# Kernel tuning notes

Hardware: AMD Instinct MI355X
Metric: run time of the kernel (lower is better)

## Reference

```python
import jax, jax.numpy as jnp
import numpy as np

B, T, N, M = 128, 128, 128, 256  # batch, timesteps, driving series, hidden size


def setup_inputs() -> dict:
    key = jax.random.key(0)
    ks = jax.random.split(key, 8)
    def p(k, shape, fan):
        return jax.random.normal(k, shape, jnp.float32) / np.float32(np.sqrt(fan))
    X = jax.random.normal(ks[0], (B, T, N), jnp.float32)
    h0 = jnp.zeros((B, M), jnp.float32)
    s0 = jnp.zeros((B, M), jnp.float32)
    Wx = p(ks[1], (N, 4 * M), N)           # LSTM input kernel (gates i,f,g,o)
    Wh = p(ks[2], (M, 4 * M), M)           # LSTM recurrent kernel
    b = jnp.zeros((4 * M,), jnp.float32)
    Wd = p(ks[3], (2 * M, T), 2 * M)       # attention W: Dense(T) on [h;s]
    bW = jnp.zeros((T,), jnp.float32)
    Ud = p(ks[4], (T, T), T)               # attention U: Dense(T) on X^T
    bU = jnp.zeros((T,), jnp.float32)
    vd = p(ks[5], (T, 1), T)               # attention v: Dense(1)
    bv = jnp.zeros((1,), jnp.float32)
    return {"X": X, "h0": h0, "s0": s0, "Wx": Wx, "Wh": Wh, "b": b,
            "Wd": Wd, "bW": bW, "Ud": Ud, "bU": bU, "vd": vd, "bv": bv}


def reference(X, h0, s0, Wx, Wh, b, Wd, bW, Ud, bU, vd, bv):
    m = h0.shape[-1]
    # U(Permute(X)) is time-invariant: precompute once. (B,N,T)
    UX = jnp.einsum('btn,tu->bnu', X, Ud) + bU

    def lstm_cell(h, c, x_t):
        z = x_t @ Wx + h @ Wh + b                      # (B,4M)
        i, f, g, o = jnp.split(z, 4, axis=-1)
        i = jax.nn.sigmoid(i)
        f = jax.nn.sigmoid(f)
        g = jnp.tanh(g)
        o = jax.nn.sigmoid(o)
        c = f * c + i * g
        h = o * jnp.tanh(c)
        return h, c

    def step(carry, x_t):
        h, c = carry
        h, c = lstm_cell(h, c, x_t)                    # (B,M),(B,M)
        hs = jnp.concatenate([h, c], axis=-1)          # (B,2M)
        w = hs @ Wd + bW                               # (B,T), broadcast over N
        e = jnp.tanh(w[:, None, :] + UX) @ vd          # (B,N,1)
        alpha = jax.nn.softmax(e[..., 0] + bv[0], axis=-1)  # softmax over N
        return (h, c), alpha

    (_, _), alphas = jax.lax.scan(step, (h0, s0), jnp.swapaxes(X, 0, 1))
    # alphas: (T,B,N) -> (B,T,N); x_tilde = alpha_t (.) x_t
    return X * jnp.swapaxes(alphas, 0, 1)
```

## Files before the change

kernel.cpp:

```cpp
#include <hip/hip_runtime.h>
#include <hip/hip_fp16.h>

#define Bc 128
#define Tc 128
#define Nc 128
#define Mc 256
#define G4 1024

typedef _Float16 half8 __attribute__((ext_vector_type(8)));
typedef float f32x4 __attribute__((ext_vector_type(4)));
typedef unsigned u32x4 __attribute__((ext_vector_type(4)));

__device__ __forceinline__ float frcp(float x) {
#if __has_builtin(__builtin_amdgcn_rcpf)
  return __builtin_amdgcn_rcpf(x);
#else
  return 1.f / x;
#endif
}
__device__ __forceinline__ float fsig(float x) { return frcp(1.f + __expf(-x)); }
__device__ __forceinline__ float ftanh(float x) {
  float t = __expf(2.f * x);
  return 1.f - 2.f * frcp(t + 1.f);
}

#define LDX4CC(dst, ptr, OFF) \
  asm volatile("global_load_dwordx4 %0, %1, off offset:" #OFF " sc0 sc1" \
               : "=v"(dst) : "v"(ptr))
#define LDX4P(dst, ptr, OFF) \
  asm volatile("global_load_dwordx4 %0, %1, off offset:" #OFF \
               : "=v"(dst) : "v"(ptr))
#define ATOMSW(ptr, v_) \
  asm volatile("global_atomic_swap %0, %1, off" :: "v"(ptr), "v"(v_) : "memory")
#define STDWP(ptr, v_) \
  asm volatile("global_store_dword %0, %1, off" :: "v"(ptr), "v"(v_) : "memory")
#define VMCNT0 do { asm volatile("s_waitcnt vmcnt(0)" ::: "memory"); \
                    __builtin_amdgcn_sched_barrier(0); } while (0)

__global__ void k_prep(const float* __restrict__ Wh, const float* __restrict__ h0,
                       __half* __restrict__ wht, unsigned* __restrict__ hx2,
                       unsigned* __restrict__ flags) {
  int bid = blockIdx.x;
  if (bid < 512) {
    int i = bid * 256 + threadIdx.x;
    int jt = i >> 11;
    int rem = i & 2047;
    int kt = rem >> 8;
    int rem2 = rem & 255;
    int lane = rem2 >> 2;
    int r2 = rem2 & 3;
    int jp = jt * 16 + (lane & 15);
    int g = jp & 3, mcol = jp >> 2;
    int j = g * 256 + mcol;
    int mk0 = kt * 32 + (lane >> 4) * 8 + r2;
    wht[(size_t)i * 2]     = __float2half(Wh[(size_t)mk0 * G4 + j]);
    wht[(size_t)i * 2 + 1] = __float2half(Wh[(size_t)(mk0 + 4) * G4 + j]);
  } else if (bid < 576) {
    int idx = (bid - 512) * 256 + threadIdx.x;
    int b = idx >> 7, i = idx & 127;
    int a = i >> 2, d = i & 3;
    unsigned lo = __half_as_ushort(__float2half(h0[(size_t)b * Mc + 8 * a + d]));
    unsigned hi = __half_as_ushort(__float2half(h0[(size_t)b * Mc + 8 * a + d + 4]));
    hx2[idx] = ~(lo | (hi << 16));
  } else if (bid < 8768) {
    int idx = (bid - 576) * 256 + threadIdx.x;
    hx2[16384 + idx] = 0u;
  } else {
    for (int i = threadIdx.x; i < 16544; i += 256) flags[i] = 0u;
    __syncthreads();
    if (threadIdx.x < 8) flags[threadIdx.x * 129 * 16] = 4u;
  }
}

__global__ void k_ux(const float* __restrict__ X, const float* __restrict__ Ud,
                     const float* __restrict__ bU, float* __restrict__ PX) {
  __shared__ float Xl[Tc][Nc];
  int b = blockIdx.x;
  const float* Xb = X + (size_t)b * Tc * Nc;
  for (int i = threadIdx.x; i < Tc * Nc; i += 256) Xl[i >> 7][i & 127] = Xb[i];
  __syncthreads();
  int n = threadIdx.x & 127;
  int uh = __builtin_amdgcn_readfirstlane(threadIdx.x >> 7);
  for (int u0 = uh * 64; u0 < uh * 64 + 64; u0 += 8) {
    float acc[8];
#pragma unroll
    for (int i = 0; i < 8; i++) acc[i] = 0.f;
    for (int tt = 0; tt < Tc; ++tt) {
      float xv = Xl[tt][n];
#pragma unroll
      for (int i = 0; i < 8; i++) acc[i] += xv * Ud[tt * Tc + u0 + i];
    }
#pragma unroll
    for (int i = 0; i < 8; i++)
      PX[((size_t)b * Tc + (u0 + i)) * Nc + n] = __expf(2.f * (acc[i] + bU[u0 + i]));
  }
}

__global__ __launch_bounds__(256, 2)
void k_xwx2(const float* __restrict__ X, const float* __restrict__ Wx,
            const float* __restrict__ bias, float* __restrict__ XWxP) {
  __shared__ float xl[32][Nc];
  int t = blockIdx.x >> 2;
  int b0 = (blockIdx.x & 3) * 32;
  for (int i = threadIdx.x; i < 32 * Nc; i += 256) {
    int row = i >> 7, n = i & 127;
    xl[row][n] = X[(size_t)(b0 + row) * Tc * Nc + (size_t)t * Nc + n];
  }
  __syncthreads();
  int m = threadIdx.x;
  float acc[32][4];
#pragma unroll
  for (int i = 0; i < 32; i++)
#pragma unroll
    for (int g = 0; g < 4; g++) acc[i][g] = 0.f;
  for (int n = 0; n < Nc; ++n) {
    float wi = Wx[(size_t)n * G4 + m];
    float wf = Wx[(size_t)n * G4 + 256 + m];
    float wg = Wx[(size_t)n * G4 + 512 + m];
    float wo = Wx[(size_t)n * G4 + 768 + m];
#pragma unroll
    for (int i = 0; i < 32; i++) {
      float xv = xl[i][n];
      acc[i][0] += xv * wi; acc[i][1] += xv * wf;
      acc[i][2] += xv * wg; acc[i][3] += xv * wo;
    }
  }
  float bi = bias[m], bf = bias[256 + m], bg = bias[512 + m], bo = bias[768 + m];
#pragma unroll
  for (int i = 0; i < 32; i++) {
    float4 o;
    o.x = acc[i][0] + bi; o.y = acc[i][1] + bf;
    o.z = acc[i][2] + bg; o.w = acc[i][3] + bo;
    *(float4*)(XWxP + ((size_t)t * Bc + b0 + i) * G4 + m * 4) = o;
  }
}

template <bool FAST>
__device__ __forceinline__ void scan_body(
    const __half* __restrict__ wht, const float* __restrict__ xwxp,
    unsigned* __restrict__ hx2, __half* __restrict__ cx,
    const float* __restrict__ s0, unsigned* __restrict__ flags,
    int q, int grp, int tid, int lane, int lg, int b, int jt0, int m0) {
  half8 A0[8], A1[8];
#pragma unroll
  for (int kt = 0; kt < 8; ++kt) {
    A0[kt] = *(const half8*)(wht + ((size_t)(jt0 * 8 + kt) * 64 + lane) * 8);
    A1[kt] = *(const half8*)(wht + ((size_t)((jt0 + 1) * 8 + kt) * 64 + lane) * 8);
  }

  float c0 = s0[(size_t)b * Mc + m0];
  float c1 = s0[(size_t)b * Mc + m0 + 4];

  const char* hq = (const char*)hx2 + ((size_t)b * 128 + lg * 4) * 4;
  char*       hs = (char*)hx2 + ((size_t)16384 + b * 128 + jt0 * 2 + lg) * 4;
  const float* xq = xwxp + ((size_t)b) * G4 + jt0 * 16 + lg * 4;
  __half*      cq = cx + (size_t)b * Mc;
  unsigned* flgp = flags + (size_t)grp * 129 * 16;

  f32x4 braw[8];

#pragma unroll 1
  for (int t = 0; t < 128; ++t) {
    asm volatile("" : "+v"(A0[0]), "+v"(A0[1]), "+v"(A0[2]), "+v"(A0[3]),
                      "+v"(A0[4]), "+v"(A0[5]), "+v"(A0[6]), "+v"(A0[7]));
    asm volatile("" : "+v"(A1[0]), "+v"(A1[1]), "+v"(A1[2]), "+v"(A1[3]),
                      "+v"(A1[4]), "+v"(A1[5]), "+v"(A1[6]), "+v"(A1[7]));

    f32x4 acc0 = *(const f32x4*)(xq);
    f32x4 acc1 = *(const f32x4*)(xq + 16);

    if (FAST) {
      if (t > 0) {
        unsigned ret = 0u;
#pragma unroll 1
        do {
          if (lane == 0)
            asm volatile("global_atomic_or %0, %1, %2, off sc0\n\t"
                         "s_waitcnt vmcnt(0)"
                         : "=v"(ret) : "v"(flgp + t * 16), "v"(0u) : "memory");
          ret = __builtin_amdgcn_readfirstlane(ret);
        } while (ret < 4u);
        __builtin_amdgcn_sched_barrier(0);
      }
      LDX4P(braw[0], hq, 0);   LDX4P(braw[1], hq, 64);
      LDX4P(braw[2], hq, 128); LDX4P(braw[3], hq, 192);
      LDX4P(braw[4], hq, 256); LDX4P(braw[5], hq, 320);
      LDX4P(braw[6], hq, 384); LDX4P(braw[7], hq, 448);
      VMCNT0;
    } else {
      LDX4CC(braw[0], hq, 0);   LDX4CC(braw[1], hq, 64);
      LDX4CC(braw[2], hq, 128); LDX4CC(braw[3], hq, 192);
      LDX4CC(braw[4], hq, 256); LDX4CC(braw[5], hq, 320);
      LDX4CC(braw[6], hq, 384); LDX4CC(braw[7], hq, 448);
      for (;;) {
        VMCNT0;
        unsigned mn = 0xFFFFFFFFu;
#pragma unroll
        for (int kt = 0; kt < 8; ++kt) {
          u32x4 u = __builtin_bit_cast(u32x4, braw[kt]);
          mn = min(mn, min(min(u.x, u.y), min(u.z, u.w)));
        }
        if (__builtin_expect(mn != 0u, 1)) break;
        LDX4CC(braw[0], hq, 0);   LDX4CC(braw[1], hq, 64);
        LDX4CC(braw[2], hq, 128); LDX4CC(braw[3], hq, 192);
        LDX4CC(braw[4], hq, 256); LDX4CC(braw[5], hq, 320);
        LDX4CC(braw[6], hq, 384); LDX4CC(braw[7], hq, 448);
      }
    }

#pragma unroll
    for (int kt = 0; kt < 8; ++kt) {
      u32x4 u = ~__builtin_bit_cast(u32x4, braw[kt]);
      half8 Bf = __builtin_bit_cast(half8, u);
      acc0 = __builtin_amdgcn_mfma_f32_16x16x32_f16(A0[kt], Bf, acc0, 0, 0, 0);
      acc1 = __builtin_amdgcn_mfma_f32_16x16x32_f16(A1[kt], Bf, acc1, 0, 0, 0);
    }
    float i0 = fsig(acc0[0]), f0 = fsig(acc0[1]);
    float g0 = ftanh(acc0[2]), o0 = fsig(acc0[3]);
    c0 = f0 * c0 + i0 * g0;
    float h0v = o0 * ftanh(c0);
    float i1 = fsig(acc1[0]), f1 = fsig(acc1[1]);
    float g1 = ftanh(acc1[2]), o1 = fsig(acc1[3]);
    c1 = f1 * c1 + i1 * g1;
    float h1v = o1 * ftanh(c1);

    unsigned pk = (unsigned)__half_as_ushort(__float2half(h0v)) |
                  ((unsigned)__half_as_ushort(__float2half(h1v)) << 16);
    if (FAST) {
      STDWP(hs, ~pk);
      cq[m0]     = __float2half(c0);
      cq[m0 + 4] = __float2half(c1);
      VMCNT0;
      __syncthreads();
      if (tid == 0)
        asm volatile("global_atomic_add %0, %1, off"
                     :: "v"(flgp + (t + 1) * 16), "v"(1u) : "memory");
    } else {
      ATOMSW(hs, ~pk);
      cq[m0]     = __float2half(c0);
      cq[m0 + 4] = __float2half(c1);
    }

    hq += 65536; hs += 65536; xq += Bc * G4; cq += Bc * Mc;
  }
}

__global__ __launch_bounds__(512, 2)
void k_scan(const __half* __restrict__ wht, const float* __restrict__ xwxp,
            unsigned* __restrict__ hx2, __half* __restrict__ cx,
            const float* __restrict__ s0, unsigned* __restrict__ flags) {
  int bid = blockIdx.x;
  int q = bid >> 3, grp = bid & 7;
  int tid = threadIdx.x;
  int lane = tid & 63;
  int lb = lane & 15, lg = lane >> 4;
  int b = grp * 16 + lb;
  int jt0 = q * 16 + (tid >> 6) * 2;
  int m0 = jt0 * 4 + lg;

  unsigned* xcdtab = flags + 16512;
  __shared__ int s_fast;
  if (tid == 0) {
    unsigned xcd;
    asm volatile("s_getreg_b32 %0, hwreg(HW_REG_XCC_ID)" : "=s"(xcd));
    asm volatile("global_store_dword %0, %1, off sc0 sc1"
                 :: "v"(xcdtab + bid), "v"(xcd + 1u) : "memory");
    unsigned ref = 0; int fast = 1;
#pragma unroll 1
    for (int k = 0; k < 4; ++k) {
      unsigned v;
      do {
        asm volatile("global_load_dword %0, %1, off sc0 sc1\n\t"
                     "s_waitcnt vmcnt(0)"
                     : "=v"(v) : "v"(xcdtab + (k * 8 + grp)) : "memory");
      } while (v == 0u);
      if (k == 0) ref = v; else fast &= (v == ref) ? 1 : 0;
    }
    s_fast = fast;
  }
  __syncthreads();

  if (s_fast)
    scan_body<true>(wht, xwxp, hx2, cx, s0, flags, q, grp, tid, lane, lg, b, jt0, m0);
  else
    scan_body<false>(wht, xwxp, hx2, cx, s0, flags, q, grp, tid, lane, lg, b, jt0, m0);
}

__global__ void k_wall2(const unsigned* __restrict__ Hxu, const __half2* __restrict__ Cx2,
                        const float* __restrict__ Wd, const float* __restrict__ bW,
                        float* __restrict__ Wall) {
  int r0 = blockIdx.x * 32;
  int wv = __builtin_amdgcn_readfirstlane(threadIdx.x >> 6);
  int lane = threadIdx.x & 63;
  int u2 = lane * 2;
  int rbase = r0 + wv * 8;
  float acc[8][2];
#pragma unroll
  for (int i = 0; i < 8; i++) { acc[i][0] = 0.f; acc[i][1] = 0.f; }
#pragma unroll 2
  for (int k2 = 0; k2 < 128; ++k2) {
    int m_lo = 8 * (k2 >> 2) + (k2 & 3);
    float2 wh0 = *(const float2*)(Wd + (size_t)m_lo * Tc + u2);
    float2 wh1 = *(const float2*)(Wd + (size_t)(m_lo + 4) * Tc + u2);
    float2 wc0 = *(const float2*)(Wd + (size_t)(Mc + 2 * k2) * Tc + u2);
    float2 wc1 = *(const float2*)(Wd + (size_t)(Mc + 2 * k2 + 1) * Tc + u2);
#pragma unroll
    for (int i = 0; i < 8; i++) {
      unsigned hraw = ~Hxu[(size_t)(rbase + i) * 128 + 16384 + k2];
      __half2 hv = __builtin_bit_cast(__half2, hraw);
      __half2 cv = Cx2[(size_t)(rbase + i) * 128 + k2];
      float hlo = __low2float(hv), hhi = __high2float(hv);
      float clo = __low2float(cv), chi = __high2float(cv);
      acc[i][0] += hlo * wh0.x + hhi * wh1.x + clo * wc0.x + chi * wc1.x;
      acc[i][1] += hlo * wh0.y + hhi * wh1.y + clo * wc0.y + chi * wc1.y;
    }
  }
  float bw0 = bW[u2], bw1 = bW[u2 + 1];
#pragma unroll
  for (int i = 0; i < 8; i++) {
    float2 o; o.x = acc[i][0] + bw0; o.y = acc[i][1] + bw1;
    *(float2*)(Wall + (size_t)(rbase + i) * Tc + u2) = o;
  }
}

__global__ void k_attn(const float* __restrict__ Wall, const float* __restrict__ PX,
                       const float* __restrict__ vd, const float* __restrict__ X,
                       float* __restrict__ out) {
  __shared__ float4 av[Nc];
  __shared__ float v2s[Nc];
  __shared__ float red[2][8];
  int b = blockIdx.x & 127, tq = blockIdx.x >> 7;
  int n = threadIdx.x;
  int wv = n >> 6;
  float4 a;
  a.x = __expf(2.f * Wall[((size_t)(tq * 4 + 0) * Bc + b) * Tc + n]);
  a.y = __expf(2.f * Wall[((size_t)(tq * 4 + 1) * Bc + b) * Tc + n]);
  a.z = __expf(2.f * Wall[((size_t)(tq * 4 + 2) * Bc + b) * Tc + n]);
  a.w = __expf(2.f * Wall[((size_t)(tq * 4 + 3) * Bc + b) * Tc + n]);
  av[n] = a;
  v2s[n] = -2.f * vd[n];
  __syncthreads();
  const float* Pb = PX + (size_t)b * Tc * Nc;
  float e0 = 0.f, e1 = 0.f, e2 = 0.f, e3 = 0.f;
#pragma unroll 4
  for (int u = 0; u < Tc; ++u) {
    float P = Pb[(size_t)u * Nc + n];
    float4 au = av[u];
    float v2 = v2s[u];
    e0 = fmaf(v2, frcp(fmaf(au.x, P, 1.f)), e0);
    e1 = fmaf(v2, frcp(fmaf(au.y, P, 1.f)), e1);
    e2 = fmaf(v2, frcp(fmaf(au.z, P, 1.f)), e2);
    e3 = fmaf(v2, frcp(fmaf(au.w, P, 1.f)), e3);
  }
  float m0 = e0, m1 = e1, m2 = e2, m3 = e3;
#pragma unroll
  for (int off = 32; off > 0; off >>= 1) {
    m0 = fmaxf(m0, __shfl_xor(m0, off));
    m1 = fmaxf(m1, __shfl_xor(m1, off));
    m2 = fmaxf(m2, __shfl_xor(m2, off));
    m3 = fmaxf(m3, __shfl_xor(m3, off));
  }
  if ((n & 63) == 0) {
    red[wv][0] = m0; red[wv][1] = m1; red[wv][2] = m2; red[wv][3] = m3;
  }
  __syncthreads();
  m0 = fmaxf(red[0][0], red[1][0]);
  m1 = fmaxf(red[0][1], red[1][1]);
  m2 = fmaxf(red[0][2], red[1][2]);
  m3 = fmaxf(red[0][3], red[1][3]);
  float x0 = __expf(e0 - m0);
  float x1 = __expf(e1 - m1);
  float x2 = __expf(e2 - m2);
  float x3 = __expf(e3 - m3);
  float s0 = x0, s1 = x1, s2 = x2, s3 = x3;
#pragma unroll
  for (int off = 32; off > 0; off >>= 1) {
    s0 += __shfl_xor(s0, off);
    s1 += __shfl_xor(s1, off);
    s2 += __shfl_xor(s2, off);
    s3 += __shfl_xor(s3, off);
  }
  if ((n & 63) == 0) {
    red[wv][4] = s0; red[wv][5] = s1; red[wv][6] = s2; red[wv][7] = s3;
  }
  __syncthreads();
  s0 = red[0][4] + red[1][4];
  s1 = red[0][5] + red[1][5];
  s2 = red[0][6] + red[1][6];
  s3 = red[0][7] + red[1][7];
  size_t xi0 = ((size_t)b * Tc + tq * 4) * Nc + n;
  out[xi0]            = X[xi0]            * (x0 * frcp(s0));
  out[xi0 + Nc]       = X[xi0 + Nc]       * (x1 * frcp(s1));
  out[xi0 + 2 * Nc]   = X[xi0 + 2 * Nc]   * (x2 * frcp(s2));
  out[xi0 + 3 * Nc]   = X[xi0 + 3 * Nc]   * (x3 * frcp(s3));
}

extern "C" void kernel_launch(void* const* d_in, const int* in_sizes, int n_in,
                              void* d_out, int out_size, void* d_ws, size_t ws_size,
                              hipStream_t stream) {
  (void)in_sizes; (void)n_in; (void)out_size; (void)ws_size;
  const float* X  = (const float*)d_in[0];
  const float* h0 = (const float*)d_in[1];
  const float* s0 = (const float*)d_in[2];
  const float* Wx = (const float*)d_in[3];
  const float* Wh = (const float*)d_in[4];
  const float* bb = (const float*)d_in[5];
  const float* Wd = (const float*)d_in[6];
  const float* bW = (const float*)d_in[7];
  const float* Ud = (const float*)d_in[8];
  const float* bU = (const float*)d_in[9];
  const float* vd = (const float*)d_in[10];
  float* out = (float*)d_out;
  float* ws = (float*)d_ws;

  float* PX       = ws;
  float* XWxP     = PX + 2097152;
  unsigned* hx2   = (unsigned*)(XWxP + 16777216);
  __half* cx      = (__half*)(hx2 + 129 * 16384);
  float* Wall     = (float*)(cx + 128 * 32768);
  __half* wht     = (__half*)(Wall + 2097152);
  unsigned* flags = (unsigned*)(wht + 262144);

  k_prep<<<8769, 256, 0, stream>>>(Wh, h0, wht, hx2, flags);
  k_ux<<<Bc, 256, 0, stream>>>(X, Ud, bU, PX);
  k_xwx2<<<Tc * 4, 256, 0, stream>>>(X, Wx, bb, XWxP);
  k_scan<<<32, 512, 0, stream>>>(wht, XWxP, hx2, cx, s0, flags);
  k_wall2<<<(Tc * Bc) / 32, 256, 0, stream>>>(hx2, (const __half2*)cx, Wd, bW, Wall);
  k_attn<<<Bc * 32, 128, 0, stream>>>(Wall, PX, vd, X, out);
}
```

Before: 644.1 us.

## Replace per-step flag polling with optimistic load and per-block done flags

In the fast same-XCD scan path, each step now loads the previous hidden state right away and checks it for the zero sentinel. Only when data is missing does it spin on four per-block done flags, then reload from a second copy of h. Each block writes h to both the main buffer and a shadow buffer and sets its own flag with an atomic swap, replacing the shared counter. The aim is to take the mandatory atomic poll round trip off the per-step critical path, at the cost of an extra store per step and a larger zero-initialised workspace.

```diff
diff --git a/kernel.cpp b/kernel.cpp
--- a/kernel.cpp
+++ b/kernel.cpp
@@ -39,7 +39,7 @@
 
 __global__ void k_prep(const float* __restrict__ Wh, const float* __restrict__ h0,
                        __half* __restrict__ wht, unsigned* __restrict__ hx2,
-                       unsigned* __restrict__ flags) {
+                       unsigned* __restrict__ hxs, unsigned* __restrict__ flags) {
   int bid = blockIdx.x;
   if (bid < 512) {
     int i = bid * 256 + threadIdx.x;
@@ -65,10 +65,12 @@
   } else if (bid < 8768) {
     int idx = (bid - 576) * 256 + threadIdx.x;
     hx2[16384 + idx] = 0u;
+  } else if (bid < 16960) {
+    int idx = (bid - 8768) * 256 + threadIdx.x;
+    hxs[idx] = 0u;
   } else {
-    for (int i = threadIdx.x; i < 16544; i += 256) flags[i] = 0u;
-    __syncthreads();
-    if (threadIdx.x < 8) flags[threadIdx.x * 129 * 16] = 4u;
+    int idx = (bid - 16960) * 256 + threadIdx.x;
+    if (idx < 66048 + 32) flags[idx] = 0u;
   }
 }
 
@@ -138,8 +140,9 @@
 template <bool FAST>
 __device__ __forceinline__ void scan_body(
     const __half* __restrict__ wht, const float* __restrict__ xwxp,
-    unsigned* __restrict__ hx2, __half* __restrict__ cx,
-    const float* __restrict__ s0, unsigned* __restrict__ flags,
+    unsigned* __restrict__ hx2, unsigned* __restrict__ hxs,
+    __half* __restrict__ cx, const float* __restrict__ s0,
+    unsigned* __restrict__ flags,
     int q, int grp, int tid, int lane, int lg, int b, int jt0, int m0) {
   half8 A0[8], A1[8];
 #pragma unroll
@@ -151,11 +154,13 @@
   float c0 = s0[(size_t)b * Mc + m0];
   float c1 = s0[(size_t)b * Mc + m0 + 4];
 
-  const char* hq = (const char*)hx2 + ((size_t)b * 128 + lg * 4) * 4;
-  char*       hs = (char*)hx2 + ((size_t)16384 + b * 128 + jt0 * 2 + lg) * 4;
+  const char* hq  = (const char*)hx2 + ((size_t)b * 128 + lg * 4) * 4;
+  const char* hq2 = (const char*)hxs + ((size_t)b * 128 + lg * 4) * 4 - 65536;
+  char*       hs  = (char*)hx2 + ((size_t)16384 + b * 128 + jt0 * 2 + lg) * 4;
+  char*       hss = (char*)hxs + ((size_t)b * 128 + jt0 * 2 + lg) * 4;
   const float* xq = xwxp + ((size_t)b) * G4 + jt0 * 16 + lg * 4;
   __half*      cq = cx + (size_t)b * Mc;
-  unsigned* flgp = flags + (size_t)grp * 129 * 16;
+  unsigned* dn = flags + (size_t)grp * 129 * 64;
 
   f32x4 braw[8];
 
@@ -170,23 +175,34 @@
     f32x4 acc1 = *(const f32x4*)(xq + 16);
 
     if (FAST) {
-      if (t > 0) {
-        unsigned ret = 0u;
-#pragma unroll 1
-        do {
-          if (lane == 0)
-            asm volatile("global_atomic_or %0, %1, %2, off sc0\n\t"
-                         "s_waitcnt vmcnt(0)"
-                         : "=v"(ret) : "v"(flgp + t * 16), "v"(0u) : "memory");
-          ret = __builtin_amdgcn_readfirstlane(ret);
-        } while (ret < 4u);
-        __builtin_amdgcn_sched_barrier(0);
-      }
       LDX4P(braw[0], hq, 0);   LDX4P(braw[1], hq, 64);
       LDX4P(braw[2], hq, 128); LDX4P(braw[3], hq, 192);
       LDX4P(braw[4], hq, 256); LDX4P(braw[5], hq, 320);
       LDX4P(braw[6], hq, 384); LDX4P(braw[7], hq, 448);
       VMCNT0;
+      unsigned mn = 0xFFFFFFFFu;
+#pragma unroll
+      for (int kt = 0; kt < 8; ++kt) {
+        u32x4 u = __builtin_bit_cast(u32x4, braw[kt]);
+        mn = min(mn, min(min(u.x, u.y), min(u.z, u.w)));
+      }
+      if (__builtin_expect(mn == 0u, 0)) {
+        unsigned v = 1u;
+#pragma unroll 1
+        do {
+          if (lane < 4)
+            asm volatile("global_atomic_or %0, %1, %2, off sc0\n\t"
+                         "s_waitcnt vmcnt(0)"
+                         : "=v"(v) : "v"(dn + (size_t)t * 64 + lane * 16), "v"(0u)
+                         : "memory");
+        } while (!__all(v == 1u));
+        __builtin_amdgcn_sched_barrier(0);
+        LDX4P(braw[0], hq2, 0);   LDX4P(braw[1], hq2, 64);
+        LDX4P(braw[2], hq2, 128); LDX4P(braw[3], hq2, 192);
+        LDX4P(braw[4], hq2, 256); LDX4P(braw[5], hq2, 320);
+        LDX4P(braw[6], hq2, 384); LDX4P(braw[7], hq2, 448);
+        VMCNT0;
+      }
     } else {
       LDX4CC(braw[0], hq, 0);   LDX4CC(braw[1], hq, 64);
       LDX4CC(braw[2], hq, 128); LDX4CC(braw[3], hq, 192);
@@ -228,27 +244,29 @@
                   ((unsigned)__half_as_ushort(__float2half(h1v)) << 16);
     if (FAST) {
       STDWP(hs, ~pk);
-      cq[m0]     = __float2half(c0);
-      cq[m0 + 4] = __float2half(c1);
+      STDWP(hss, ~pk);
       VMCNT0;
       __syncthreads();
       if (tid == 0)
-        asm volatile("global_atomic_add %0, %1, off"
-                     :: "v"(flgp + (t + 1) * 16), "v"(1u) : "memory");
+        ATOMSW(dn + (size_t)(t + 1) * 64 + q * 16, 1u);
+      cq[m0]     = __float2half(c0);
+      cq[m0 + 4] = __float2half(c1);
     } else {
       ATOMSW(hs, ~pk);
       cq[m0]     = __float2half(c0);
       cq[m0 + 4] = __float2half(c1);
     }
 
-    hq += 65536; hs += 65536; xq += Bc * G4; cq += Bc * Mc;
+    hq += 65536; hq2 += 65536; hs += 65536; hss += 65536;
+    xq += Bc * G4; cq += Bc * Mc;
   }
 }
 
 __global__ __launch_bounds__(512, 2)
 void k_scan(const __half* __restrict__ wht, const float* __restrict__ xwxp,
-            unsigned* __restrict__ hx2, __half* __restrict__ cx,
-            const float* __restrict__ s0, unsigned* __restrict__ flags) {
+            unsigned* __restrict__ hx2, unsigned* __restrict__ hxs,
+            __half* __restrict__ cx, const float* __restrict__ s0,
+            unsigned* __restrict__ flags) {
   int bid = blockIdx.x;
   int q = bid >> 3, grp = bid & 7;
   int tid = threadIdx.x;
@@ -258,7 +276,7 @@
   int jt0 = q * 16 + (tid >> 6) * 2;
   int m0 = jt0 * 4 + lg;
 
-  unsigned* xcdtab = flags + 16512;
+  unsigned* xcdtab = flags + 66048;
   __shared__ int s_fast;
   if (tid == 0) {
     unsigned xcd;
@@ -281,9 +299,9 @@
   __syncthreads();
 
   if (s_fast)
-    scan_body<true>(wht, xwxp, hx2, cx, s0, flags, q, grp, tid, lane, lg, b, jt0, m0);
+    scan_body<true>(wht, xwxp, hx2, hxs, cx, s0, flags, q, grp, tid, lane, lg, b, jt0, m0);
   else
-    scan_body<false>(wht, xwxp, hx2, cx, s0, flags, q, grp, tid, lane, lg, b, jt0, m0);
+    scan_body<false>(wht, xwxp, hx2, hxs, cx, s0, flags, q, grp, tid, lane, lg, b, jt0, m0);
 }
 
 __global__ void k_wall2(const unsigned* __restrict__ Hxu, const __half2* __restrict__ Cx2,
@@ -416,15 +434,16 @@
   float* PX       = ws;
   float* XWxP     = PX + 2097152;
   unsigned* hx2   = (unsigned*)(XWxP + 16777216);
-  __half* cx      = (__half*)(hx2 + 129 * 16384);
+  unsigned* hxs   = hx2 + 129 * 16384;
+  __half* cx      = (__half*)(hxs + 128 * 16384);
   float* Wall     = (float*)(cx + 128 * 32768);
   __half* wht     = (__half*)(Wall + 2097152);
   unsigned* flags = (unsigned*)(wht + 262144);
 
-  k_prep<<<8769, 256, 0, stream>>>(Wh, h0, wht, hx2, flags);
+  k_prep<<<17219, 256, 0, stream>>>(Wh, h0, wht, hx2, hxs, flags);
   k_ux<<<Bc, 256, 0, stream>>>(X, Ud, bU, PX);
   k_xwx2<<<Tc * 4, 256, 0, stream>>>(X, Wx, bb, XWxP);
-  k_scan<<<32, 512, 0, stream>>>(wht, XWxP, hx2, cx, s0, flags);
+  k_scan<<<32, 512, 0, stream>>>(wht, XWxP, hx2, hxs, cx, s0, flags);
   k_wall2<<<(Tc * Bc) / 32, 256, 0, stream>>>(hx2, (const __half2*)cx, Wd, bW, Wall);
   k_attn<<<Bc * 32, 128, 0, stream>>>(Wall, PX, vd, X, out);
 }
```

New measurement: 685.9 us. 1.07x slower.

## Fuse LSTM input projection into recurrent scan via fp16 MFMA

Applied to the files above, without the earlier changes.

Removes the separate k_xwx2 kernel and its large fp32 precomputed X·Wx buffer. Wx is instead pre-packed to fp16 in MFMA-friendly layout, X is packed per timestep, and each scan step computes the input contribution with four extra MFMA pairs seeded with the bias. The aim is to cut a whole kernel and the heavy global write and read of the gate pre-activation buffer. The trade-offs are lower precision for the input GEMM, more registers per thread (launch bounds relaxed to one block per CU), and extra compute on the serial critical path. The c-state stores are also moved after the step-completion flag is signalled.

```diff
diff --git a/kernel.cpp b/kernel.cpp
--- a/kernel.cpp
+++ b/kernel.cpp
@@ -37,8 +37,10 @@
 #define VMCNT0 do { asm volatile("s_waitcnt vmcnt(0)" ::: "memory"); \
                     __builtin_amdgcn_sched_barrier(0); } while (0)
 
-__global__ void k_prep(const float* __restrict__ Wh, const float* __restrict__ h0,
-                       __half* __restrict__ wht, unsigned* __restrict__ hx2,
+__global__ void k_prep(const float* __restrict__ Wh, const float* __restrict__ Wx,
+                       const float* __restrict__ X, const float* __restrict__ h0,
+                       __half* __restrict__ wht, __half* __restrict__ wxt,
+                       __half* __restrict__ xtp, unsigned* __restrict__ hx2,
                        unsigned* __restrict__ flags) {
   int bid = blockIdx.x;
   if (bid < 512) {
@@ -55,20 +57,45 @@
     int mk0 = kt * 32 + (lane >> 4) * 8 + r2;
     wht[(size_t)i * 2]     = __float2half(Wh[(size_t)mk0 * G4 + j]);
     wht[(size_t)i * 2 + 1] = __float2half(Wh[(size_t)(mk0 + 4) * G4 + j]);
-  } else if (bid < 576) {
-    int idx = (bid - 512) * 256 + threadIdx.x;
+  } else if (bid < 768) {
+    int i = (bid - 512) * 256 + threadIdx.x;
+    int jt = i >> 10;
+    int rem = i & 1023;
+    int kt = rem >> 8;
+    int rem2 = rem & 255;
+    int lane = rem2 >> 2;
+    int r2 = rem2 & 3;
+    int jp = jt * 16 + (lane & 15);
+    int g = jp & 3, mcol = jp >> 2;
+    int j = g * 256 + mcol;
+    int n0 = kt * 32 + (lane >> 4) * 8 + 2 * r2;
+    wxt[(size_t)i * 2]     = __float2half(Wx[(size_t)n0 * G4 + j]);
+    wxt[(size_t)i * 2 + 1] = __float2half(Wx[(size_t)(n0 + 1) * G4 + j]);
+  } else if (bid < 832) {
+    int idx = (bid - 768) * 256 + threadIdx.x;
     int b = idx >> 7, i = idx & 127;
     int a = i >> 2, d = i & 3;
     unsigned lo = __half_as_ushort(__float2half(h0[(size_t)b * Mc + 8 * a + d]));
     unsigned hi = __half_as_ushort(__float2half(h0[(size_t)b * Mc + 8 * a + d + 4]));
     hx2[idx] = ~(lo | (hi << 16));
-  } else if (bid < 8768) {
-    int idx = (bid - 576) * 256 + threadIdx.x;
+  } else if (bid < 9024) {
+    int idx = (bid - 832) * 256 + threadIdx.x;
     hx2[16384 + idx] = 0u;
+  } else if (bid < 13120) {
+    int i = (bid - 9024) * 256 + threadIdx.x;
+    int t = i >> 13;
+    int rem = i & 8191;
+    int b = rem >> 6;
+    int rem2 = rem & 63;
+    int kt = rem2 >> 4;
+    int r = rem2 & 15;
+    int lg = r >> 2, r2 = r & 3;
+    int n0 = kt * 32 + lg * 8 + 2 * r2;
+    const float* xr = X + ((size_t)b * Tc + t) * Nc;
+    xtp[(size_t)i * 2]     = __float2half(xr[n0]);
+    xtp[(size_t)i * 2 + 1] = __float2half(xr[n0 + 1]);
   } else {
     for (int i = threadIdx.x; i < 16544; i += 256) flags[i] = 0u;
-    __syncthreads();
-    if (threadIdx.x < 8) flags[threadIdx.x * 129 * 16] = 4u;
   }
 }
 
@@ -96,50 +123,13 @@
   }
 }
 
-__global__ __launch_bounds__(256, 2)
-void k_xwx2(const float* __restrict__ X, const float* __restrict__ Wx,
-            const float* __restrict__ bias, float* __restrict__ XWxP) {
-  __shared__ float xl[32][Nc];
-  int t = blockIdx.x >> 2;
-  int b0 = (blockIdx.x & 3) * 32;
-  for (int i = threadIdx.x; i < 32 * Nc; i += 256) {
-    int row = i >> 7, n = i & 127;
-    xl[row][n] = X[(size_t)(b0 + row) * Tc * Nc + (size_t)t * Nc + n];
-  }
-  __syncthreads();
-  int m = threadIdx.x;
-  float acc[32][4];
-#pragma unroll
-  for (int i = 0; i < 32; i++)
-#pragma unroll
-    for (int g = 0; g < 4; g++) acc[i][g] = 0.f;
-  for (int n = 0; n < Nc; ++n) {
-    float wi = Wx[(size_t)n * G4 + m];
-    float wf = Wx[(size_t)n * G4 + 256 + m];
-    float wg = Wx[(size_t)n * G4 + 512 + m];
-    float wo = Wx[(size_t)n * G4 + 768 + m];
-#pragma unroll
-    for (int i = 0; i < 32; i++) {
-      float xv = xl[i][n];
-      acc[i][0] += xv * wi; acc[i][1] += xv * wf;
-      acc[i][2] += xv * wg; acc[i][3] += xv * wo;
-    }
-  }
-  float bi = bias[m], bf = bias[256 + m], bg = bias[512 + m], bo = bias[768 + m];
-#pragma unroll
-  for (int i = 0; i < 32; i++) {
-    float4 o;
-    o.x = acc[i][0] + bi; o.y = acc[i][1] + bf;
-    o.z = acc[i][2] + bg; o.w = acc[i][3] + bo;
-    *(float4*)(XWxP + ((size_t)t * Bc + b0 + i) * G4 + m * 4) = o;
-  }
-}
-
 template <bool FAST>
 __device__ __forceinline__ void scan_body(
-    const __half* __restrict__ wht, const float* __restrict__ xwxp,
+    const __half* __restrict__ wht, const __half* __restrict__ wxt,
+    const __half* __restrict__ xtp,
     unsigned* __restrict__ hx2, __half* __restrict__ cx,
-    const float* __restrict__ s0, unsigned* __restrict__ flags,
+    const float* __restrict__ s0, const float* __restrict__ bb,
+    unsigned* __restrict__ flags,
     int q, int grp, int tid, int lane, int lg, int b, int jt0, int m0) {
   half8 A0[8], A1[8];
 #pragma unroll
@@ -147,17 +137,29 @@
     A0[kt] = *(const half8*)(wht + ((size_t)(jt0 * 8 + kt) * 64 + lane) * 8);
     A1[kt] = *(const half8*)(wht + ((size_t)((jt0 + 1) * 8 + kt) * 64 + lane) * 8);
   }
+  half8 Ax0[4], Ax1[4];
+#pragma unroll
+  for (int kt = 0; kt < 4; ++kt) {
+    Ax0[kt] = *(const half8*)(wxt + ((size_t)(jt0 * 4 + kt) * 64 + lane) * 8);
+    Ax1[kt] = *(const half8*)(wxt + ((size_t)((jt0 + 1) * 4 + kt) * 64 + lane) * 8);
+  }
+  f32x4 binit0, binit1;
+  binit0[0] = bb[m0];       binit0[1] = bb[256 + m0];
+  binit0[2] = bb[512 + m0]; binit0[3] = bb[768 + m0];
+  binit1[0] = bb[m0 + 4];       binit1[1] = bb[256 + m0 + 4];
+  binit1[2] = bb[512 + m0 + 4]; binit1[3] = bb[768 + m0 + 4];
 
   float c0 = s0[(size_t)b * Mc + m0];
   float c1 = s0[(size_t)b * Mc + m0 + 4];
 
   const char* hq = (const char*)hx2 + ((size_t)b * 128 + lg * 4) * 4;
   char*       hs = (char*)hx2 + ((size_t)16384 + b * 128 + jt0 * 2 + lg) * 4;
-  const float* xq = xwxp + ((size_t)b) * G4 + jt0 * 16 + lg * 4;
+  const char* xt = (const char*)xtp + (size_t)b * 256 + lg * 16;
   __half*      cq = cx + (size_t)b * Mc;
   unsigned* flgp = flags + (size_t)grp * 129 * 16;
 
   f32x4 braw[8];
+  f32x4 bx0, bx1, bx2, bx3;
 
 #pragma unroll 1
   for (int t = 0; t < 128; ++t) {
@@ -165,9 +167,11 @@
                       "+v"(A0[4]), "+v"(A0[5]), "+v"(A0[6]), "+v"(A0[7]));
     asm volatile("" : "+v"(A1[0]), "+v"(A1[1]), "+v"(A1[2]), "+v"(A1[3]),
                       "+v"(A1[4]), "+v"(A1[5]), "+v"(A1[6]), "+v"(A1[7]));
-
-    f32x4 acc0 = *(const f32x4*)(xq);
-    f32x4 acc1 = *(const f32x4*)(xq + 16);
+    asm volatile("" : "+v"(Ax0[0]), "+v"(Ax0[1]), "+v"(Ax0[2]), "+v"(Ax0[3]),
+                      "+v"(Ax1[0]), "+v"(Ax1[1]), "+v"(Ax1[2]), "+v"(Ax1[3]),
+                      "+v"(binit0), "+v"(binit1));
+
+    LDX4P(bx0, xt, 0); LDX4P(bx1, xt, 64); LDX4P(bx2, xt, 128); LDX4P(bx3, xt, 192);
 
     if (FAST) {
       if (t > 0) {
@@ -208,6 +212,21 @@
       }
     }
 
+    f32x4 acc0 = binit0, acc1 = binit1;
+    {
+      half8 B0 = __builtin_bit_cast(half8, bx0);
+      half8 B1 = __builtin_bit_cast(half8, bx1);
+      half8 B2 = __builtin_bit_cast(half8, bx2);
+      half8 B3 = __builtin_bit_cast(half8, bx3);
+      acc0 = __builtin_amdgcn_mfma_f32_16x16x32_f16(Ax0[0], B0, acc0, 0, 0, 0);
+      acc1 = __builtin_amdgcn_mfma_f32_16x16x32_f16(Ax1[0], B0, acc1, 0, 0, 0);
+      acc0 = __builtin_amdgcn_mfma_f32_16x16x32_f16(Ax0[1], B1, acc0, 0, 0, 0);
+      acc1 = __builtin_amdgcn_mfma_f32_16x16x32_f16(Ax1[1], B1, acc1, 0, 0, 0);
+      acc0 = __builtin_amdgcn_mfma_f32_16x16x32_f16(Ax0[2], B2, acc0, 0, 0, 0);
+      acc1 = __builtin_amdgcn_mfma_f32_16x16x32_f16(Ax1[2], B2, acc1, 0, 0, 0);
+      acc0 = __builtin_amdgcn_mfma_f32_16x16x32_f16(Ax0[3], B3, acc0, 0, 0, 0);
+      acc1 = __builtin_amdgcn_mfma_f32_16x16x32_f16(Ax1[3], B3, acc1, 0, 0, 0);
+    }
 #pragma unroll
     for (int kt = 0; kt < 8; ++kt) {
       u32x4 u = ~__builtin_bit_cast(u32x4, braw[kt]);
@@ -228,27 +247,29 @@
                   ((unsigned)__half_as_ushort(__float2half(h1v)) << 16);
     if (FAST) {
       STDWP(hs, ~pk);
-      cq[m0]     = __float2half(c0);
-      cq[m0 + 4] = __float2half(c1);
       VMCNT0;
       __syncthreads();
       if (tid == 0)
         asm volatile("global_atomic_add %0, %1, off"
                      :: "v"(flgp + (t + 1) * 16), "v"(1u) : "memory");
+      cq[m0]     = __float2half(c0);
+      cq[m0 + 4] = __float2half(c1);
     } else {
       ATOMSW(hs, ~pk);
       cq[m0]     = __float2half(c0);
       cq[m0 + 4] = __float2half(c1);
     }
 
-    hq += 65536; hs += 65536; xq += Bc * G4; cq += Bc * Mc;
-  }
-}
-
-__global__ __launch_bounds__(512, 2)
-void k_scan(const __half* __restrict__ wht, const float* __restrict__ xwxp,
+    hq += 65536; hs += 65536; xt += 32768; cq += Bc * Mc;
+  }
+}
+
+__global__ __launch_bounds__(512, 1)
+void k_scan(const __half* __restrict__ wht, const __half* __restrict__ wxt,
+            const __half* __restrict__ xtp,
             unsigned* __restrict__ hx2, __half* __restrict__ cx,
-            const float* __restrict__ s0, unsigned* __restrict__ flags) {
+            const float* __restrict__ s0, const float* __restrict__ bb,
+            unsigned* __restrict__ flags) {
   int bid = blockIdx.x;
   int q = bid >> 3, grp = bid & 7;
   int tid = threadIdx.x;
@@ -281,9 +302,9 @@
   __syncthreads();
 
   if (s_fast)
-    scan_body<true>(wht, xwxp, hx2, cx, s0, flags, q, grp, tid, lane, lg, b, jt0, m0);
+    scan_body<true>(wht, wxt, xtp, hx2, cx, s0, bb, flags, q, grp, tid, lane, lg, b, jt0, m0);
   else
-    scan_body<false>(wht, xwxp, hx2, cx, s0, flags, q, grp, tid, lane, lg, b, jt0, m0);
+    scan_body<false>(wht, wxt, xtp, hx2, cx, s0, bb, flags, q, grp, tid, lane, lg, b, jt0, m0);
 }
 
 __global__ void k_wall2(const unsigned* __restrict__ Hxu, const __half2* __restrict__ Cx2,
@@ -414,17 +435,17 @@
   float* ws = (float*)d_ws;
 
   float* PX       = ws;
-  float* XWxP     = PX + 2097152;
-  unsigned* hx2   = (unsigned*)(XWxP + 16777216);
+  unsigned* hx2   = (unsigned*)(PX + 2097152);
   __half* cx      = (__half*)(hx2 + 129 * 16384);
   float* Wall     = (float*)(cx + 128 * 32768);
   __half* wht     = (__half*)(Wall + 2097152);
-  unsigned* flags = (unsigned*)(wht + 262144);
-
-  k_prep<<<8769, 256, 0, stream>>>(Wh, h0, wht, hx2, flags);
+  __half* wxt     = wht + 262144;
+  __half* xtp     = wxt + 131072;
+  unsigned* flags = (unsigned*)(xtp + 2097152);
+
+  k_prep<<<13121, 256, 0, stream>>>(Wh, Wx, X, h0, wht, wxt, xtp, hx2, flags);
   k_ux<<<Bc, 256, 0, stream>>>(X, Ud, bU, PX);
-  k_xwx2<<<Tc * 4, 256, 0, stream>>>(X, Wx, bb, XWxP);
-  k_scan<<<32, 512, 0, stream>>>(wht, XWxP, hx2, cx, s0, flags);
+  k_scan<<<32, 512, 0, stream>>>(wht, wxt, xtp, hx2, cx, s0, bb, flags);
   k_wall2<<<(Tc * Bc) / 32, 256, 0, stream>>>(hx2, (const __half2*)cx, Wd, bW, Wall);
   k_attn<<<Bc * 32, 128, 0, stream>>>(Wall, PX, vd, X, out);
 }
```

Measured after the change: 644.9 us. About the same (+0.1%).
